# Kernel optimization log

Hardware: AMD Instinct MI355X
Metric: run time of the kernel (lower is better)

## Reference

```python
import jax, jax.numpy as jnp
import numpy as np

N = 50000      # n_points (== n_support, non-strided)
H = 32         # neighbors per point
IN_F = 128
OUT_F = 256
MID = OUT_F // 4   # bottleneck width = 64
K = 15         # kernel points
RADIUS = 2.0
KP_EXTENT = 1.2 * RADIUS / 5.0  # config.KP_extent * radius / density_parameter
EPS = 1e-6
SLOPE = 0.1


def _wvar(k, size):
    # weight_variable: normal(scale=sqrt(2/size[-1])), zeroed outside 2*std
    std = np.sqrt(2.0 / size[-1])
    w = jax.random.normal(k, size, jnp.float32) * std
    return jnp.where(jnp.abs(w) > 2.0 * std, 0.0, w)


def setup_inputs():
    key = jax.random.key(0)
    ks = jax.random.split(key, 12)
    query_points = jax.random.uniform(ks[0], (N, 3), jnp.float32)
    support_points = query_points  # non-strided: same cloud
    neighbors_indices = jax.random.randint(ks[1], (N, H), 0, N, jnp.int32)
    features = jax.random.normal(ks[2], (N, IN_F), jnp.float32)
    kp = (jax.random.uniform(ks[3], (K, 3), jnp.float32) * 2.0 - 1.0) * (0.66 * KP_EXTENT)
    kernel_points = kp.at[0].set(0.0)  # fixed_kernel_points='center'
    w1 = _wvar(ks[4], (IN_F, MID))
    kw = _wvar(ks[5], (K, MID, MID))
    w3 = _wvar(ks[6], (MID, OUT_F))
    ws = _wvar(ks[7], (IN_F, OUT_F))
    def bnp(k, c):
        k1, k2 = jax.random.split(k)
        g = jax.random.uniform(k1, (c,), jnp.float32, 0.75, 1.25)
        b = jax.random.normal(k2, (c,), jnp.float32) * 0.1
        return g, b
    g1, b1 = bnp(ks[8], MID)
    g2, b2 = bnp(ks[9], MID)
    g3, b3 = bnp(ks[10], OUT_F)
    gs, bs = bnp(ks[11], OUT_F)
    return dict(query_points=query_points, support_points=support_points,
                neighbors_indices=neighbors_indices, features=features,
                kernel_points=kernel_points, w1=w1, g1=g1, b1=b1,
                kw=kw, g2=g2, b2=b2, w3=w3, g3=g3, b3=b3, ws=ws, gs=gs, bs=bs)


def _bn(x, g, b):
    # BatchNorm1d in training mode: batch statistics over points, biased var
    m = jnp.mean(x, 0)
    v = jnp.var(x, 0)
    return g * (x - m) * jax.lax.rsqrt(v + EPS) + b


def _lrelu(x):
    return jnp.where(x >= 0, x, SLOPE * x)


def _unary(x, w, g, b):
    return _lrelu(_bn(x @ w, g, b))


def _kpconv(q, s, inds, f, kp, kw):
    # pad support with a far shadow point and features with a zero row (faithful to KPConv)
    s_pad = jnp.concatenate([s, jnp.full((1, 3), 1e6, s.dtype)], 0)
    f_pad = jnp.concatenate([f, jnp.zeros((1, f.shape[1]), f.dtype)], 0)
    neigh = s_pad[inds]                        # [n,h,3] gather
    d = neigh - q[:, None, :]                  # [n,h,3]
    sq = jnp.sum((d[:, :, None, :] - kp[None, None, :, :]) ** 2, -1)  # [n,h,K]
    dist = jnp.sqrt(jnp.maximum(sq, 1e-12))
    infl = jnp.maximum(0.0, 1.0 - dist / KP_EXTENT)   # 'linear' KP_influence
    nf = f_pad[inds]                           # [n,h,d] gather
    wf = jnp.einsum('nhk,nhd->nkd', infl, nf)  # aggregate over neighbors
    return jnp.einsum('nkd,kdo->no', wf, kw)   # 'sum' aggregation over kernel pts


def reference(query_points, support_points, neighbors_indices, features, kernel_points,
              w1, g1, b1, kw, g2, b2, w3, g3, b3, ws, gs, bs):
    x = _unary(features, w1, g1, b1)                                     # conv1
    x = _lrelu(_bn(_kpconv(query_points, support_points, neighbors_indices,
                           x, kernel_points, kw), g2, b2))               # conv2 (KPConv)
    x = _unary(x, w3, g3, b3)                                            # conv3
    sc = _unary(features, ws, gs, bs)                                    # shortcut (non-strided)
    return _lrelu(sc + x)
```

## Files before the change

### kernel.cpp

```cpp
#include <hip/hip_runtime.h>

#define NPTS 50000
#define HN 32
#define INF1 128
#define OUTF3 256
#define MIDF 64
#define KP 15
#define EPSV 1e-6f
#define SLOPE 0.1f
#define KPE 0.48f
#define INVN (1.f / 50000.f)

typedef __attribute__((ext_vector_type(8))) short short8;
typedef __attribute__((ext_vector_type(4))) float float4v;
typedef unsigned short ushort;
typedef unsigned long long ull;

__device__ inline ushort f2bf(float f) {
    union { float f; unsigned u; } v; v.f = f;
    unsigned r = v.u + 0x7fff + ((v.u >> 16) & 1);
    return (ushort)(r >> 16);
}
__device__ inline float bf2f(ushort u) {
    union { unsigned u; float f; } v; v.u = ((unsigned)u) << 16;
    return v.f;
}
__device__ inline unsigned cvt_pk_bf16(float lo, float hi) {
    unsigned r;
    asm("v_cvt_pk_bf16_f32 %0, %1, %2" : "=v"(r) : "v"(lo), "v"(hi));
    return r;
}


__global__ __launch_bounds__(256)
void k_repack_all(const float* __restrict__ w1, const float* __restrict__ wsw,
                  ushort* __restrict__ wpC,
                  const float* __restrict__ kw, ushort* __restrict__ wpk,
                  const float* __restrict__ w3, ushort* __restrict__ wp3) {
    int id = blockIdx.x * 256 + threadIdx.x;
    if (id < 5120) {
        int l = id & 63;
        int nt = (id >> 6) % 20, s = id / 1280;
        int n = nt * 16 + (l & 15);
        int k0 = s * 32 + ((l >> 4) & 3) * 8;
#pragma unroll
        for (int j = 0; j < 8; j++) {
            float v = (n < 64) ? w1[(k0 + j) * 64 + n] : wsw[(k0 + j) * 256 + (n - 64)];
            wpC[id * 8 + j] = f2bf(v);
        }
    } else if (id < 13312) {
        int id2 = id - 5120;
        int l2 = id2 & 63;
        int nt = (id2 >> 6) & 3, s = id2 >> 8;
        int n = nt * 16 + (l2 & 15);
        int kd0 = s * 32 + ((l2 >> 4) & 3) * 8;
#pragma unroll
        for (int j = 0; j < 8; j++) {
            int kd = kd0 + j, d = kd >> 4, kk = kd & 15;
            float v = (kk < KP) ? kw[kk * 4096 + d * 64 + n] : 0.f;
            wpk[id2 * 8 + j] = f2bf(v);
        }
    } else if (id < 15360) {
        int id3 = id - 13312;
        int l3 = id3 & 63;
        int nt = (id3 >> 6) % 16, s = id3 / 1024;
        int n = nt * 16 + (l3 & 15);
        int k0 = s * 32 + ((l3 >> 4) & 3) * 8;
#pragma unroll
        for (int j = 0; j < 8; j++)
            wp3[id3 * 8 + j] = f2bf(w3[(k0 + j) * 256 + n]);
    }
}

__global__ __launch_bounds__(256)
void k_conv1sc(const float* __restrict__ feat, const ushort* __restrict__ WpC,
               ushort* __restrict__ x1raw, ushort* __restrict__ scb,
               float* __restrict__ Sa1, float* __restrict__ Sq1,
               float* __restrict__ SaS, float* __restrict__ SqS, int M) {
    __shared__ float sred[320], qred[320];
    int t = threadIdx.x;
    int w = t >> 6, l = t & 63;
    int dl = l & 15, q4 = l >> 4;

    for (int c = t; c < 320; c += 256) { sred[c] = 0.f; qred[c] = 0.f; }
    __syncthreads();

    int m0 = blockIdx.x * 64 + w * 16;
    int row = m0 + dl;
    long arow = (row < M) ? row : (M - 1);
    const float* ap0 = feat + arow * INF1 + q4 * 8;
    short8 afr[4];
#pragma unroll
    for (int s = 0; s < 4; s++) {
        float4 a0 = *(const float4*)(ap0 + s * 32);
        float4 a1 = *(const float4*)(ap0 + s * 32 + 4);
        union { short8 v; unsigned d[4]; } au;
        au.d[0] = cvt_pk_bf16(a0.x, a0.y);
        au.d[1] = cvt_pk_bf16(a0.z, a0.w);
        au.d[2] = cvt_pk_bf16(a1.x, a1.y);
        au.d[3] = cvt_pk_bf16(a1.z, a1.w);
        afr[s] = au.v;
    }
    const short8* Bp = (const short8*)WpC + l;
    int rb = q4 * 4;
#pragma unroll
    for (int half = 0; half < 2; half++) {
        float4v acc[10];
#pragma unroll
        for (int j = 0; j < 10; j++) acc[j] = (float4v){0.f, 0.f, 0.f, 0.f};
#pragma unroll
        for (int s = 0; s < 4; s++)
#pragma unroll
            for (int j = 0; j < 10; j++) {
                short8 bf = Bp[(s * 20 + half * 10 + j) * 64];
                acc[j] = __builtin_amdgcn_mfma_f32_16x16x32_bf16(afr[s], bf, acc[j], 0, 0, 0);
            }
#pragma unroll
        for (int r = 0; r < 4; r++) {
            int rr = m0 + rb + r;
            if (rr < M) {
                if (half == 0) {
                    uint2 pk;
                    pk.x = cvt_pk_bf16(acc[0][r], acc[1][r]);
                    pk.y = cvt_pk_bf16(acc[2][r], acc[3][r]);
                    *(uint2*)(x1raw + (long)rr * 64 + 4 * dl) = pk;
#pragma unroll
                    for (int j = 4; j < 10; j++)
                        scb[(long)rr * 256 + (j * 16 + dl - 64)] = f2bf(acc[j][r]);
                } else {
#pragma unroll
                    for (int j = 0; j < 10; j++)
                        scb[(long)rr * 256 + ((10 + j) * 16 + dl - 64)] = f2bf(acc[j][r]);
                }
            }
        }
#pragma unroll
        for (int j = 0; j < 10; j++) {
            float s = 0.f, q = 0.f;
#pragma unroll
            for (int r = 0; r < 4; r++) {
                float v = ((m0 + rb + r) < M) ? acc[j][r] : 0.f;
                s += v; q += v * v;
            }
            s += __shfl_xor(s, 16); s += __shfl_xor(s, 32);
            q += __shfl_xor(q, 16); q += __shfl_xor(q, 32);
            if (q4 == 0) {
                atomicAdd(&sred[(half * 10 + j) * 16 + dl], s);
                atomicAdd(&qred[(half * 10 + j) * 16 + dl], q);
            }
        }
    }
    __syncthreads();
    for (int c = t; c < 320; c += 256) {
        if (c < 64) { atomicAdd(&Sa1[c], sred[c]); atomicAdd(&Sq1[c], qred[c]); }
        else        { atomicAdd(&SaS[c - 64], sred[c]); atomicAdd(&SqS[c - 64], qred[c]); }
    }
}

__global__ __launch_bounds__(256)
void k_bnx(const ushort* __restrict__ X, ushort* __restrict__ Y,
           const float* __restrict__ Sa, const float* __restrict__ Sq,
           const float* __restrict__ g, const float* __restrict__ b) {
    __shared__ float sc[64], sh[64];
    int t = threadIdx.x;
    if (t < 64) {
        float m = Sa[t] * INVN;
        float v = Sq[t] * INVN - m * m;
        float s = g[t] * rsqrtf(v + EPSV);
        sc[t] = s; sh[t] = b[t] - s * m;
    }
    __syncthreads();
    int i = blockIdx.x * 256 + t;
    long base = (long)i * 4;
    int dlp = i & 15;
    ull vin = *(const ull*)(X + base);
    float vv[4];
#pragma unroll
    for (int j = 0; j < 4; j++) {
        int c = j * 16 + dlp;
        float f = bf2f((ushort)((vin >> (16 * j)) & 0xffff));
        float v = f * sc[c] + sh[c];
        vv[j] = (v >= 0.f) ? v : SLOPE * v;
    }
    uint2 vo;
    vo.x = cvt_pk_bf16(vv[0], vv[1]);
    vo.y = cvt_pk_bf16(vv[2], vv[3]);
    *(uint2*)(Y + base) = vo;
}

__global__ __launch_bounds__(256)
void k_kpconv(const float* __restrict__ qpts, const float* __restrict__ spts,
              const int* __restrict__ nbr, const ushort* __restrict__ x1b,
              const float* __restrict__ kpp, const ushort* __restrict__ kwp,
              ushort* __restrict__ y, float* __restrict__ Sa, float* __restrict__ Sq) {
    __shared__ __align__(16) ushort wfs[16][1032];
    __shared__ float posd[4][4][3][HN];

    int t = threadIdx.x;
    int w = t >> 6, l = t & 63;
    int dl = l & 15, q4 = l >> 4;

    int kmin = (dl < KP) ? dl : (KP - 1);
    float kx = kpp[kmin * 3 + 0], ky = kpp[kmin * 3 + 1], kz = kpp[kmin * 3 + 2];

    int nb = blockIdx.x * 16 + w * 4;

    int idg[4][8];
#pragma unroll
    for (int pp = 0; pp < 4; pp++) {
        const int4* np = (const int4*)(nbr + (long)(nb + pp) * HN + q4 * 8);
        int4 ia = np[0], ib = np[1];
        idg[pp][0] = ia.x; idg[pp][1] = ia.y; idg[pp][2] = ia.z; idg[pp][3] = ia.w;
        idg[pp][4] = ib.x; idg[pp][5] = ib.y; idg[pp][6] = ib.z; idg[pp][7] = ib.w;
    }

    {
        int hh = l & 31, hf = l >> 5;
        float dx[2], dy[2], dz[2];
#pragma unroll
        for (int p2 = 0; p2 < 2; p2++) {
            int pp = hf * 2 + p2;
            int idx = nbr[(long)(nb + pp) * HN + hh];
            dx[p2] = spts[(long)idx * 3 + 0] - qpts[(nb + pp) * 3 + 0];
            dy[p2] = spts[(long)idx * 3 + 1] - qpts[(nb + pp) * 3 + 1];
            dz[p2] = spts[(long)idx * 3 + 2] - qpts[(nb + pp) * 3 + 2];
        }
#pragma unroll
        for (int p2 = 0; p2 < 2; p2++) {
            int pp = hf * 2 + p2;
            posd[w][pp][0][hh] = dx[p2];
            posd[w][pp][1][hh] = dy[p2];
            posd[w][pp][2][hh] = dz[p2];
        }
    }

    uint2 rj[4][8];
#pragma unroll
    for (int pp = 0; pp < 4; pp++)
#pragma unroll
        for (int j = 0; j < 8; j++)
            rj[pp][j] = *(const uint2*)(x1b + (long)idg[pp][j] * MIDF + 4 * dl);

#pragma unroll
    for (int pp = 0; pp < 4; pp++) {
        union { float4 v; float f[4]; } px0, px1, py0, py1, pz0, pz1;
        px0.v = *(const float4*)&posd[w][pp][0][q4 * 8];
        px1.v = *(const float4*)&posd[w][pp][0][q4 * 8 + 4];
        py0.v = *(const float4*)&posd[w][pp][1][q4 * 8];
        py1.v = *(const float4*)&posd[w][pp][1][q4 * 8 + 4];
        pz0.v = *(const float4*)&posd[w][pp][2][q4 * 8];
        pz1.v = *(const float4*)&posd[w][pp][2][q4 * 8 + 4];

        float inf[8];
#pragma unroll
        for (int j = 0; j < 8; j++) {
            float ex = ((j < 4) ? px0.f[j & 3] : px1.f[j & 3]) - kx;
            float ey = ((j < 4) ? py0.f[j & 3] : py1.f[j & 3]) - ky;
            float ez = ((j < 4) ? pz0.f[j & 3] : pz1.f[j & 3]) - kz;
            float sq = ex * ex + ey * ey + ez * ez;
            float dist = sqrtf(fmaxf(sq, 1e-12f));
            inf[j] = fmaxf(0.f, 1.f - dist * (1.f / KPE));
        }
        union { short8 v; unsigned d2[4]; } afr;
#pragma unroll
        for (int jj = 0; jj < 4; jj++)
            afr.d2[jj] = cvt_pk_bf16(inf[2 * jj], inf[2 * jj + 1]);

        union { short8 v; unsigned d[4]; } bfr[4];
#pragma unroll
        for (int dj = 0; dj < 4; dj++) {
            unsigned a_lo = rj[pp][2 * dj].x, b_lo = rj[pp][2 * dj + 1].x;
            unsigned a_hi = rj[pp][2 * dj].y, b_hi = rj[pp][2 * dj + 1].y;
            bfr[0].d[dj] = __builtin_amdgcn_perm(b_lo, a_lo, 0x05040100u);
            bfr[1].d[dj] = __builtin_amdgcn_perm(b_lo, a_lo, 0x07060302u);
            bfr[2].d[dj] = __builtin_amdgcn_perm(b_hi, a_hi, 0x05040100u);
            bfr[3].d[dj] = __builtin_amdgcn_perm(b_hi, a_hi, 0x07060302u);
        }

        float4v wfa[4];
#pragma unroll
        for (int nt = 0; nt < 4; nt++)
            wfa[nt] = __builtin_amdgcn_mfma_f32_16x16x32_bf16(
                afr.v, bfr[nt].v, (float4v){0.f, 0.f, 0.f, 0.f}, 0, 0, 0);

        int p = w * 4 + pp;
#pragma unroll
        for (int nt = 0; nt < 4; nt++) {
            uint2 pk;
            pk.x = cvt_pk_bf16(wfa[nt][0], wfa[nt][1]);
            pk.y = cvt_pk_bf16(wfa[nt][2], wfa[nt][3]);
            *(uint2*)(&wfs[p][(nt * 16 + dl) * 16 + q4 * 4]) = pk;
        }
    }

    const short8* Bq = (const short8*)kwp + l;
    short8 bc0 = Bq[(0 * 4 + w) * 64];
    short8 bc1 = Bq[(1 * 4 + w) * 64];
    __syncthreads();

    float4v acc0 = (float4v){0.f, 0.f, 0.f, 0.f};
    float4v acc1 = (float4v){0.f, 0.f, 0.f, 0.f};
    const ushort* arow = &wfs[dl][0] + q4 * 8;
#pragma unroll
    for (int s = 0; s < 32; s += 2) {
        short8 bn0, bn1;
        if (s < 30) {
            bn0 = Bq[((s + 2) * 4 + w) * 64];
            bn1 = Bq[((s + 3) * 4 + w) * 64];
        }
        short8 a0 = *(const short8*)(arow + s * 32);
        short8 a1 = *(const short8*)(arow + (s + 1) * 32);
        acc0 = __builtin_amdgcn_mfma_f32_16x16x32_bf16(a0, bc0, acc0, 0, 0, 0);
        acc1 = __builtin_amdgcn_mfma_f32_16x16x32_bf16(a1, bc1, acc1, 0, 0, 0);
        bc0 = bn0; bc1 = bn1;
    }
    float4v acc = acc0 + acc1;

    int o = w * 16 + dl;
    float s = 0.f, q = 0.f;
#pragma unroll
    for (int r = 0; r < 4; r++) {
        float v = acc[r];
        y[(long)(blockIdx.x * 16 + q4 * 4 + r) * MIDF + o] = f2bf(v);
        s += v; q += v * v;
    }
    s += __shfl_xor(s, 16); s += __shfl_xor(s, 32);
    q += __shfl_xor(q, 16); q += __shfl_xor(q, 32);
    if (q4 == 0) {
        atomicAdd(&Sa[o], s);
        atomicAdd(&Sq[o], q);
    }
}

__global__ __launch_bounds__(256)
void k_conv3stats(const ushort* __restrict__ x2raw, const ushort* __restrict__ Wp,
                  const float* __restrict__ Sa2, const float* __restrict__ Sq2,
                  const float* __restrict__ g2, const float* __restrict__ b2,
                  float* __restrict__ Sa3, float* __restrict__ Sq3, int M) {
    __shared__ float sred[256], qred[256];
    __shared__ float scs[64], shs[64];
    int t = threadIdx.x;
    int w = t >> 6, l = t & 63;
    int dl = l & 15, q4 = l >> 4;

    if (t < 64) {
        float m = Sa2[t] * INVN;
        float v = Sq2[t] * INVN - m * m;
        float s = g2[t] * rsqrtf(v + EPSV);
        scs[t] = s; shs[t] = b2[t] - s * m;
    }
    sred[t] = 0.f; qred[t] = 0.f;
    __syncthreads();

    int m0 = blockIdx.x * 64 + w * 16;
    int row = m0 + dl;
    long arow = (row < M) ? row : (M - 1);
    const ushort* ap0 = x2raw + arow * MIDF + q4 * 8;
    short8 au2[2];
#pragma unroll
    for (int s = 0; s < 2; s++) {
        union { short8 v; ushort u[8]; } raw;
        union { short8 v; unsigned d[4]; } cv;
        raw.v = *(const short8*)(ap0 + s * 32);
        float fv[8];
#pragma unroll
        for (int e = 0; e < 8; e++) {
            int d = s * 32 + q4 * 8 + e;
            float f = bf2f(raw.u[e]) * scs[d] + shs[d];
            fv[e] = (f >= 0.f) ? f : SLOPE * f;
        }
#pragma unroll
        for (int e2 = 0; e2 < 4; e2++)
            cv.d[e2] = cvt_pk_bf16(fv[2 * e2], fv[2 * e2 + 1]);
        au2[s] = cv.v;
    }
    const short8* Bp = (const short8*)Wp + l;
    int rb = q4 * 4;
#pragma unroll
    for (int half = 0; half < 2; half++) {
        float4v acc[8];
#pragma unroll
        for (int j = 0; j < 8; j++) acc[j] = (float4v){0.f, 0.f, 0.f, 0.f};
#pragma unroll
        for (int s = 0; s < 2; s++)
#pragma unroll
            for (int j = 0; j < 8; j++) {
                short8 bf = Bp[(s * 16 + half * 8 + j) * 64];
                acc[j] = __builtin_amdgcn_mfma_f32_16x16x32_bf16(au2[s], bf, acc[j], 0, 0, 0);
            }
#pragma unroll
        for (int j = 0; j < 8; j++) {
            float s = 0.f, q = 0.f;
#pragma unroll
            for (int r = 0; r < 4; r++) {
                float v = ((m0 + rb + r) < M) ? acc[j][r] : 0.f;
                s += v; q += v * v;
            }
            s += __shfl_xor(s, 16); s += __shfl_xor(s, 32);
            q += __shfl_xor(q, 16); q += __shfl_xor(q, 32);
            if (q4 == 0) {
                atomicAdd(&sred[(half * 8 + j) * 16 + dl], s);
                atomicAdd(&qred[(half * 8 + j) * 16 + dl], q);
            }
        }
    }
    __syncthreads();
    atomicAdd(&Sa3[t], sred[t]);
    atomicAdd(&Sq3[t], qred[t]);
}

__global__ __launch_bounds__(256)
void k_conv3final(const ushort* __restrict__ x2raw, const ushort* __restrict__ Wp,
                  const ushort* __restrict__ scb, float* __restrict__ out,
                  const float* __restrict__ Sa2, const float* __restrict__ Sq2,
                  const float* __restrict__ g2, const float* __restrict__ b2,
                  const float* __restrict__ a3, const float* __restrict__ q3,
                  const float* __restrict__ g3, const float* __restrict__ b3,
                  const float* __restrict__ aS, const float* __restrict__ qS,
                  const float* __restrict__ gs, const float* __restrict__ bs,
                  int M) {
    __shared__ float scs[64], shs[64];
    __shared__ float s3[256], h3[256], sS[256], hS[256];
    __shared__ __align__(8) ushort x3t[64][256];
    int t = threadIdx.x;
    int w = t >> 6, l = t & 63;
    int dl = l & 15, q4 = l >> 4;

    if (t < 64) {
        float m = Sa2[t] * INVN;
        float v = Sq2[t] * INVN - m * m;
        float s = g2[t] * rsqrtf(v + EPSV);
        scs[t] = s; shs[t] = b2[t] - s * m;
    }
    {
        float m = a3[t] * INVN;
        float v = q3[t] * INVN - m * m;
        float s = g3[t] * rsqrtf(v + EPSV);
        s3[t] = s; h3[t] = b3[t] - s * m;
        m = aS[t] * INVN;
        v = qS[t] * INVN - m * m;
        s = gs[t] * rsqrtf(v + EPSV);
        sS[t] = s; hS[t] = bs[t] - s * m;
    }
    __syncthreads();

    int m0 = blockIdx.x * 64 + w * 16;
    int row = m0 + dl;
    long arow = (row < M) ? row : (M - 1);
    const ushort* ap0 = x2raw + arow * MIDF + q4 * 8;
    short8 au2[2];
#pragma unroll
    for (int s = 0; s < 2; s++) {
        union { short8 v; ushort u[8]; } raw;
        union { short8 v; unsigned d[4]; } cv;
        raw.v = *(const short8*)(ap0 + s * 32);
        float fv[8];
#pragma unroll
        for (int e = 0; e < 8; e++) {
            int d = s * 32 + q4 * 8 + e;
            float f = bf2f(raw.u[e]) * scs[d] + shs[d];
            fv[e] = (f >= 0.f) ? f : SLOPE * f;
        }
#pragma unroll
        for (int e2 = 0; e2 < 4; e2++)
            cv.d[e2] = cvt_pk_bf16(fv[2 * e2], fv[2 * e2 + 1]);
        au2[s] = cv.v;
    }
    const short8* Bp = (const short8*)Wp + l;
    int rb = q4 * 4;
#pragma unroll
    for (int half = 0; half < 2; half++) {
        float4v acc[8];
#pragma unroll
        for (int j = 0; j < 8; j++) acc[j] = (float4v){0.f, 0.f, 0.f, 0.f};
#pragma unroll
        for (int s = 0; s < 2; s++)
#pragma unroll
            for (int j = 0; j < 8; j++) {
                short8 bf = Bp[(s * 16 + half * 8 + j) * 64];
                acc[j] = __builtin_amdgcn_mfma_f32_16x16x32_bf16(au2[s], bf, acc[j], 0, 0, 0);
            }
#pragma unroll
        for (int r = 0; r < 4; r++) {
            int lrow = w * 16 + rb + r;
#pragma unroll
            for (int j = 0; j < 8; j++)
                x3t[lrow][(half * 8 + j) * 16 + dl] = f2bf(acc[j][r]);
        }
    }
    __syncthreads();

#pragma unroll
    for (int it = 0; it < 16; it++) {
        int e = it * 1024 + t * 4;
        int lrow = e >> 8;
        int grow = blockIdx.x * 64 + lrow;
        if (grow < M) {
            int col = e & 255;
            ull va = *(const ull*)&x3t[lrow][col];
            ull vb = *(const ull*)(scb + (long)grow * 256 + col);
            float r[4];
#pragma unroll
            for (int j = 0; j < 4; j++) {
                int c = col + j;
                float x = bf2f((ushort)((va >> (16 * j)) & 0xffff)) * s3[c] + h3[c];
                x = (x >= 0.f) ? x : SLOPE * x;
                float sc = bf2f((ushort)((vb >> (16 * j)) & 0xffff)) * sS[c] + hS[c];
                sc = (sc >= 0.f) ? sc : SLOPE * sc;
                float v = x + sc;
                r[j] = (v >= 0.f) ? v : SLOPE * v;
            }
            *(float4*)(out + (long)grow * 256 + col) = (float4){r[0], r[1], r[2], r[3]};
        }
    }
}

extern "C" void kernel_launch(void* const* d_in, const int* in_sizes, int n_in,
                              void* d_out, int out_size, void* d_ws, size_t ws_size,
                              hipStream_t stream) {
    const float* qp   = (const float*)d_in[0];
    const float* sp   = (const float*)d_in[1];
    const int*   nbr  = (const int*)d_in[2];
    const float* feat = (const float*)d_in[3];
    const float* kpp  = (const float*)d_in[4];
    const float* w1   = (const float*)d_in[5];
    const float* g1   = (const float*)d_in[6];
    const float* b1   = (const float*)d_in[7];
    const float* kw   = (const float*)d_in[8];
    const float* g2   = (const float*)d_in[9];
    const float* b2   = (const float*)d_in[10];
    const float* w3   = (const float*)d_in[11];
    const float* g3   = (const float*)d_in[12];
    const float* b3   = (const float*)d_in[13];
    const float* wsw  = (const float*)d_in[14];
    const float* gs   = (const float*)d_in[15];
    const float* bs   = (const float*)d_in[16];
    float* out = (float*)d_out;

    char* base = (char*)d_ws;
    ushort* x1raw = (ushort*)(base + 0);
    ushort* x1b   = (ushort*)(base + 6400000);
    ushort* x2raw = (ushort*)(base + 12800000);
    ushort* scb   = (ushort*)(base + 44800000);
    ushort* wpC   = (ushort*)(base + 70400000);
    ushort* wpk   = (ushort*)(base + 70481920);
    ushort* wp3   = (ushort*)(base + 70612992);
    float*  st    = (float*)(base + 70645760);
    float* acc1 = st,       *q1 = st + 64;
    float* acc2 = st + 128, *q2 = st + 192;
    float* acc3 = st + 256, *q3 = st + 512;
    float* accS = st + 768, *qS = st + 1024;

    hipMemsetAsync(st, 0, 1280 * sizeof(float), stream);

    k_repack_all<<<60, 256, 0, stream>>>(w1, wsw, wpC, kw, wpk, w3, wp3);

    k_conv1sc<<<782, 256, 0, stream>>>(feat, wpC, x1raw, scb, acc1, q1, accS, qS, NPTS);
    k_bnx<<<3125, 256, 0, stream>>>(x1raw, x1b, acc1, q1, g1, b1);

    k_kpconv<<<NPTS / 16, 256, 0, stream>>>(qp, sp, nbr, x1b, kpp, wpk, x2raw, acc2, q2);

    k_conv3stats<<<782, 256, 0, stream>>>(x2raw, wp3, acc2, q2, g2, b2, acc3, q3, NPTS);
    k_conv3final<<<782, 256, 0, stream>>>(x2raw, wp3, scb, out,
                                          acc2, q2, g2, b2, acc3, q3,
                                          g3, b3, accS, qS, gs, bs, NPTS);
}
```

Measured before the change: 298.3 us.

## Fuse conv1 BN+LeakyReLU into KPConv gather and fold stats memset into repack

Removes the standalone k_bnx pass that normalized x1 into a separate buffer. KPConv now computes the BN1 scale and shift per block and applies BN+LeakyReLU to each gathered neighbor row before building the MFMA operands. The memset of the statistics buffer is folded into an extra block of the repack kernel. This saves one kernel launch plus a full read/write of x1, but repeats the normalization for every gathered neighbor (32x redundant ALU work) inside the KPConv inner loop.

```diff
diff --git a/kernel.cpp b/kernel.cpp
--- a/kernel.cpp
+++ b/kernel.cpp
@@ -25,6 +25,9 @@
     union { unsigned u; float f; } v; v.u = ((unsigned)u) << 16;
     return v.f;
 }
+__device__ inline float u2f(unsigned u) {
+    union { unsigned u; float f; } v; v.u = u; return v.f;
+}
 __device__ inline unsigned cvt_pk_bf16(float lo, float hi) {
     unsigned r;
     asm("v_cvt_pk_bf16_f32 %0, %1, %2" : "=v"(r) : "v"(lo), "v"(hi));
@@ -36,7 +39,8 @@
 void k_repack_all(const float* __restrict__ w1, const float* __restrict__ wsw,
                   ushort* __restrict__ wpC,
                   const float* __restrict__ kw, ushort* __restrict__ wpk,
-                  const float* __restrict__ w3, ushort* __restrict__ wp3) {
+                  const float* __restrict__ w3, ushort* __restrict__ wp3,
+                  float* __restrict__ st) {
     int id = blockIdx.x * 256 + threadIdx.x;
     if (id < 5120) {
         int l = id & 63;
@@ -69,6 +73,9 @@
 #pragma unroll
         for (int j = 0; j < 8; j++)
             wp3[id3 * 8 + j] = f2bf(w3[(k0 + j) * 256 + n]);
+    } else {
+        int c = id - 15360;
+        for (int k = c; k < 1280; k += 256) st[k] = 0.f;
     }
 }
 
@@ -158,47 +165,30 @@
 }
 
 __global__ __launch_bounds__(256)
-void k_bnx(const ushort* __restrict__ X, ushort* __restrict__ Y,
-           const float* __restrict__ Sa, const float* __restrict__ Sq,
-           const float* __restrict__ g, const float* __restrict__ b) {
-    __shared__ float sc[64], sh[64];
-    int t = threadIdx.x;
-    if (t < 64) {
-        float m = Sa[t] * INVN;
-        float v = Sq[t] * INVN - m * m;
-        float s = g[t] * rsqrtf(v + EPSV);
-        sc[t] = s; sh[t] = b[t] - s * m;
-    }
-    __syncthreads();
-    int i = blockIdx.x * 256 + t;
-    long base = (long)i * 4;
-    int dlp = i & 15;
-    ull vin = *(const ull*)(X + base);
-    float vv[4];
-#pragma unroll
-    for (int j = 0; j < 4; j++) {
-        int c = j * 16 + dlp;
-        float f = bf2f((ushort)((vin >> (16 * j)) & 0xffff));
-        float v = f * sc[c] + sh[c];
-        vv[j] = (v >= 0.f) ? v : SLOPE * v;
-    }
-    uint2 vo;
-    vo.x = cvt_pk_bf16(vv[0], vv[1]);
-    vo.y = cvt_pk_bf16(vv[2], vv[3]);
-    *(uint2*)(Y + base) = vo;
-}
-
-__global__ __launch_bounds__(256)
 void k_kpconv(const float* __restrict__ qpts, const float* __restrict__ spts,
-              const int* __restrict__ nbr, const ushort* __restrict__ x1b,
+              const int* __restrict__ nbr, const ushort* __restrict__ x1raw,
               const float* __restrict__ kpp, const ushort* __restrict__ kwp,
-              ushort* __restrict__ y, float* __restrict__ Sa, float* __restrict__ Sq) {
+              ushort* __restrict__ y, float* __restrict__ Sa, float* __restrict__ Sq,
+              const float* __restrict__ Sa1, const float* __restrict__ Sq1,
+              const float* __restrict__ g1, const float* __restrict__ b1) {
     __shared__ __align__(16) ushort wfs[16][1032];
     __shared__ float posd[4][4][3][HN];
+    __shared__ float sc1[64], sh1[64];
 
     int t = threadIdx.x;
     int w = t >> 6, l = t & 63;
     int dl = l & 15, q4 = l >> 4;
+
+    if (t < 64) {
+        float m = Sa1[t] * INVN;
+        float v = Sq1[t] * INVN - m * m;
+        float s = g1[t] * rsqrtf(v + EPSV);
+        sc1[t] = s; sh1[t] = b1[t] - s * m;
+    }
+    __syncthreads();
+    float scl[4], shl[4];
+#pragma unroll
+    for (int j = 0; j < 4; j++) { scl[j] = sc1[j * 16 + dl]; shl[j] = sh1[j * 16 + dl]; }
 
     int kmin = (dl < KP) ? dl : (KP - 1);
     float kx = kpp[kmin * 3 + 0], ky = kpp[kmin * 3 + 1], kz = kpp[kmin * 3 + 2];
@@ -239,7 +229,7 @@
     for (int pp = 0; pp < 4; pp++)
 #pragma unroll
         for (int j = 0; j < 8; j++)
-            rj[pp][j] = *(const uint2*)(x1b + (long)idg[pp][j] * MIDF + 4 * dl);
+            rj[pp][j] = *(const uint2*)(x1raw + (long)idg[pp][j] * MIDF + 4 * dl);
 
 #pragma unroll
     for (int pp = 0; pp < 4; pp++) {
@@ -266,11 +256,26 @@
         for (int jj = 0; jj < 4; jj++)
             afr.d2[jj] = cvt_pk_bf16(inf[2 * jj], inf[2 * jj + 1]);
 
+        uint2 rb8[8];
+#pragma unroll
+        for (int j = 0; j < 8; j++) {
+            unsigned lo = rj[pp][j].x, hi = rj[pp][j].y;
+            float v0 = u2f(lo << 16)          * scl[0] + shl[0];
+            float v1 = u2f(lo & 0xffff0000u)  * scl[1] + shl[1];
+            float v2 = u2f(hi << 16)          * scl[2] + shl[2];
+            float v3 = u2f(hi & 0xffff0000u)  * scl[3] + shl[3];
+            v0 = (v0 >= 0.f) ? v0 : SLOPE * v0;
+            v1 = (v1 >= 0.f) ? v1 : SLOPE * v1;
+            v2 = (v2 >= 0.f) ? v2 : SLOPE * v2;
+            v3 = (v3 >= 0.f) ? v3 : SLOPE * v3;
+            rb8[j].x = cvt_pk_bf16(v0, v1);
+            rb8[j].y = cvt_pk_bf16(v2, v3);
+        }
         union { short8 v; unsigned d[4]; } bfr[4];
 #pragma unroll
         for (int dj = 0; dj < 4; dj++) {
-            unsigned a_lo = rj[pp][2 * dj].x, b_lo = rj[pp][2 * dj + 1].x;
-            unsigned a_hi = rj[pp][2 * dj].y, b_hi = rj[pp][2 * dj + 1].y;
+            unsigned a_lo = rb8[2 * dj].x, b_lo = rb8[2 * dj + 1].x;
+            unsigned a_hi = rb8[2 * dj].y, b_hi = rb8[2 * dj + 1].y;
             bfr[0].d[dj] = __builtin_amdgcn_perm(b_lo, a_lo, 0x05040100u);
             bfr[1].d[dj] = __builtin_amdgcn_perm(b_lo, a_lo, 0x07060302u);
             bfr[2].d[dj] = __builtin_amdgcn_perm(b_hi, a_hi, 0x05040100u);
@@ -539,7 +544,6 @@
 
     char* base = (char*)d_ws;
     ushort* x1raw = (ushort*)(base + 0);
-    ushort* x1b   = (ushort*)(base + 6400000);
     ushort* x2raw = (ushort*)(base + 12800000);
     ushort* scb   = (ushort*)(base + 44800000);
     ushort* wpC   = (ushort*)(base + 70400000);
@@ -551,14 +555,12 @@
     float* acc3 = st + 256, *q3 = st + 512;
     float* accS = st + 768, *qS = st + 1024;
 
-    hipMemsetAsync(st, 0, 1280 * sizeof(float), stream);
-
-    k_repack_all<<<60, 256, 0, stream>>>(w1, wsw, wpC, kw, wpk, w3, wp3);
+    k_repack_all<<<61, 256, 0, stream>>>(w1, wsw, wpC, kw, wpk, w3, wp3, st);
 
     k_conv1sc<<<782, 256, 0, stream>>>(feat, wpC, x1raw, scb, acc1, q1, accS, qS, NPTS);
-    k_bnx<<<3125, 256, 0, stream>>>(x1raw, x1b, acc1, q1, g1, b1);
-
-    k_kpconv<<<NPTS / 16, 256, 0, stream>>>(qp, sp, nbr, x1b, kpp, wpk, x2raw, acc2, q2);
+
+    k_kpconv<<<NPTS / 16, 256, 0, stream>>>(qp, sp, nbr, x1raw, kpp, wpk, x2raw,
+                                            acc2, q2, acc1, q1, g1, b1);
 
     k_conv3stats<<<782, 256, 0, stream>>>(x2raw, wp3, acc2, q2, g2, b2, acc3, q3, NPTS);
     k_conv3final<<<782, 256, 0, stream>>>(x2raw, wp3, scb, out,
```

Result: no change. 296.6 us (median of 2 runs) (-0.6%).
